# Optimization experiments

Hardware: AMD Instinct MI355X
Metric: run time of the kernel (lower is better)

## Reference

```python
import jax, jax.numpy as jnp
import numpy as np

B, T, IN_DIM, OUT_DIM = 1024, 64, 8, 2
H, K, HIDDEN = 3, 5, 256
LOG_STD_MIN, LOG_STD_MAX = -20.0, 2.0


def setup_inputs() -> dict:
    key = jax.random.key(0)
    ks = jax.random.split(key, 12)
    def lin(k, fan_in, fan_out):
        b = 1.0 / np.sqrt(fan_in)
        return jax.random.uniform(k, (fan_in, fan_out), jnp.float32, -b, b)
    inp = {
        'state': jax.random.normal(ks[0], (B, T, IN_DIM), jnp.float32),
        'noise': jax.random.normal(ks[1], (B, T, OUT_DIM), jnp.float32),
        'Wq': lin(ks[2], IN_DIM, K * H),
        'Wk': lin(ks[3], K, K * H),
        'Wv': lin(ks[4], K, K * H),
        'W1': lin(ks[5], K * H + IN_DIM, HIDDEN),
        'b1': jnp.zeros((HIDDEN,), jnp.float32),
        'W2': lin(ks[6], HIDDEN, HIDDEN),
        'b2': jnp.zeros((HIDDEN,), jnp.float32),
        'Wmu': jax.random.uniform(ks[7], (HIDDEN, OUT_DIM), jnp.float32, -0.003, 0.003),
        'bmu': jax.random.uniform(ks[8], (OUT_DIM,), jnp.float32, -0.003, 0.003),
        'Wls': jax.random.uniform(ks[9], (HIDDEN, OUT_DIM), jnp.float32, -0.003, 0.003),
        'bls': jax.random.uniform(ks[10], (OUT_DIM,), jnp.float32, -0.003, 0.003),
    }
    return inp


# static off-diagonal neighbor indices: row i -> all j != i
_OFFDIAG = np.array([[j for j in range(T) if j != i] for i in range(T)], dtype=np.int32)


def _forward(state, noise, Wq, Wk, Wv, W1, b1, W2, b2, Wmu, bmu, Wls, bls):
    b, t, _ = state.shape
    # rel[b,i,j] = state[b,j,:4] - state[b,i,:4]
    rel4 = state[:, None, :, 0:4] - state[:, :, None, 0:4]          # [b,t,t,4] (x,y,vx,vy)
    x_comp = rel4[..., 0::2]                                         # [x, vx]
    y_comp = rel4[..., 1::2]                                         # [y, vy]
    ang = (-state[:, :, 7] + 0.5 * jnp.pi)[:, None, :, None]         # varies with j (own-ref of key agent)
    c, s = jnp.cos(ang), jnp.sin(ang)
    xn = x_comp * c - y_comp * s                                     # [x', vx']
    yn = x_comp * s + y_comp * c                                     # [y', vy']
    rel = jnp.stack([xn[..., 0], yn[..., 0], xn[..., 1], yn[..., 1]], axis=-1)  # [b,t,t,4]
    # drop self-pairs (diagonal) -> [b,t,t-1,4]
    idx = jnp.asarray(_OFFDIAG)
    rel_od = rel[:, jnp.arange(t)[:, None], idx]
    r = jnp.sqrt(rel_od[..., 0] ** 2 + rel_od[..., 1] ** 2)[..., None]   # [b,t,t-1,1]
    r_trans = jax.nn.sigmoid(1.0 - 5.0 * (r - 0.2))                       # 1/(1+exp(-1+5(r-0.2)))
    rel_n = jnp.concatenate([rel_od[..., 0:2] / r, rel_od[..., 2:4], r_trans], axis=-1)  # [b,t,t-1,5]
    h, k = H, K
    q = (state @ Wq).reshape(b, t, h, k)                              # [b,t,h,k]
    keys = (rel_n @ Wk).reshape(b, t, t - 1, h, k)                    # [b,t,n,h,k]
    vals = (rel_n @ Wv).reshape(b, t, t - 1, h, k)
    scores = jnp.einsum('btnhk,bthk->bthn', keys, q) / jnp.sqrt(jnp.float32(k))
    w = jax.nn.softmax(scores, axis=-1)                               # over t-1 neighbors
    att = jnp.einsum('bthn,btnhk->bthk', w, vals).reshape(b, t, h * k)
    x = jnp.concatenate([att, state], axis=-1)
    x = jax.nn.relu(x @ W1 + b1)
    x = jax.nn.relu(x @ W2 + b2)
    mu = jnp.tanh(x @ Wmu + bmu)
    log_std = jnp.tanh(x @ Wls + bls)
    log_std = LOG_STD_MIN + 0.5 * (LOG_STD_MAX - LOG_STD_MIN) * (log_std + 1.0)
    std = jnp.exp(log_std)
    z = mu + std * noise                                              # rsample with explicit noise
    action = jnp.tanh(z)
    # Normal(mu,std).log_prob(z) with (z-mu)/std == noise
    log_prob = -0.5 * noise ** 2 - log_std - 0.5 * jnp.log(2.0 * jnp.pi)
    log_prob = log_prob - jnp.log(1.0 - action ** 2 + 1e-7)
    log_prob = jnp.sum(log_prob, axis=-1, keepdims=True)
    return action, log_prob


def reference(state, noise, Wq, Wk, Wv, W1, b1, W2, b2, Wmu, bmu, Wls, bls):
    return _forward(state, noise, Wq, Wk, Wv, W1, b1, W2, b2, Wmu, bmu, Wls, bls)
```

## Files before the change

kernel.cpp:

```cpp
#include <hip/hip_runtime.h>
#include <math.h>

#define NROWS 65536

typedef short bf16x8 __attribute__((ext_vector_type(8)));
typedef float f32x4  __attribute__((ext_vector_type(4)));
typedef float f32x2  __attribute__((ext_vector_type(2)));
typedef unsigned int u32x2 __attribute__((ext_vector_type(2)));

__device__ __forceinline__ unsigned short f2bf(float x){
    unsigned int u = __float_as_uint(x);
    u += 0x7FFFu + ((u >> 16) & 1u);
    return (unsigned short)(u >> 16);
}
__device__ __forceinline__ unsigned int pkbf(float lo, float hi){
    unsigned int r;
    asm("v_cvt_pk_bf16_f32 %0, %1, %2" : "=v"(r) : "v"(lo), "v"(hi));
    return r;
}
__device__ __forceinline__ f32x2 sp2(float x){ return (f32x2){x, x}; }

template<int CTRL, int RM>
__device__ __forceinline__ float dpp_add(float v){
    int m = __builtin_amdgcn_update_dpp(0, __float_as_int(v), CTRL, RM, 0xF, 1);
    return v + __int_as_float(m);
}
__device__ __forceinline__ float bfly8_add(float v){
    v = dpp_add<0xB1, 0xF>(v);
    v = dpp_add<0x4E, 0xF>(v);
    v = dpp_add<0x141, 0xF>(v);
    return v;
}
__device__ __forceinline__ float red4_lq(float v){
    v += __int_as_float(__builtin_amdgcn_ds_swizzle(__float_as_int(v), 0x401F));
    v += __shfl_xor(v, 32, 64);
    return v;
}
__device__ __forceinline__ float fast_tanh(float x){
    float e = __builtin_amdgcn_exp2f(x * 2.8853900817779268f);
    return 1.f - 2.f * __builtin_amdgcn_rcpf(e + 1.f);
}

__global__ __launch_bounds__(256) void prep_kernel(
    const float* __restrict__ W2, const float* __restrict__ W1,
    unsigned short* __restrict__ w2frag, unsigned short* __restrict__ w1frag)
{
    const int bx = blockIdx.x, t = threadIdx.x;
    if (bx < 128){
        const int ct = bx >> 3, kk = bx & 7;
        #pragma unroll
        for (int s = 0; s < 2; ++s){
            int f = t * 2 + s;
            int lane = f >> 3, e = f & 7;
            int k = kk * 32 + (lane >> 4) * 8 + e;
            int c = ct * 16 + (lane & 15);
            w2frag[(size_t)(ct * 8 + kk) * 512 + f] = f2bf(W2[k * 256 + c]);
        }
    } else {
        #pragma unroll
        for (int s = 0; s < 32; ++s){
            int flat = t * 32 + s;
            int ct = flat >> 9, r = flat & 511;
            int lane = r >> 3, e = r & 7;
            int k = (lane >> 4) * 8 + e;
            int c = ct * 16 + (lane & 15);
            w1frag[flat] = (k < 23) ? f2bf(W1[k * 256 + c]) : (unsigned short)0;
        }
    }
}

__global__ __launch_bounds__(512, 4) void actor_kernel(
    const float* __restrict__ state, const float* __restrict__ noise,
    const float* __restrict__ Wq, const float* __restrict__ Wk,
    const float* __restrict__ Wv,
    const unsigned short* __restrict__ w1frag, const float* __restrict__ b1,
    const unsigned short* __restrict__ w2frag, const float* __restrict__ b2,
    const float* __restrict__ Wmu, const float* __restrict__ bmu,
    const float* __restrict__ Wls, const float* __restrict__ bls,
    float* __restrict__ action_out, float* __restrict__ logprob_out)
{
    __shared__ __align__(16) unsigned char uniA[64 * 264 * 2];
    float* sLDS  = (float*)uniA;
    float* pjLDS = sLDS + 576;
    float* qkLDS = pjLDS + 384;
    unsigned short* h1LDS = (unsigned short*)uniA;
    __shared__ __align__(16) unsigned short x0LDS[64 * 40];
    __shared__ __align__(16) float headLDS[8 * 64 * 4];

    const int t    = threadIdx.x;
    const int lane = t & 63;
    const int w    = t >> 6;
    const int lm   = lane & 15;
    const int lq   = lane >> 4;
    const int b    = blockIdx.x;

    {
        float v = state[(size_t)b * 512 + t];
        int r = t >> 3, c = t & 7;
        sLDS[r * 9 + c] = v;
        if (c < 4) pjLDS[(r & 31) * 12 + c * 2 + (r >> 5)] = v;
    }
    __syncthreads();

    if (t < 192){
        const int row = t & 63, h = t >> 6;
        float s[8];
        #pragma unroll
        for (int d = 0; d < 8; ++d) s[d] = sLDS[row * 9 + d];
        float q[5];
        #pragma unroll
        for (int e = 0; e < 5; ++e){
            int m = h * 5 + e;
            float acc = 0.f;
            #pragma unroll
            for (int d = 0; d < 8; ++d) acc += s[d] * Wq[d * 15 + m];
            q[e] = acc;
        }
        #pragma unroll
        for (int f = 0; f < 5; ++f){
            float acc = 0.f;
            #pragma unroll
            for (int kk = 0; kk < 5; ++kk) acc += Wk[f * 15 + h * 5 + kk] * q[kk];
            qkLDS[row * 20 + h * 5 + f] = acc * 0.64519834f;
        }
    } else if (w == 7){
        const int row = lane;
        float ang = 1.5707963267948966f - sLDS[row * 9 + 7];
        float sn, cs;
        __sincosf(ang, &sn, &cs);
        int base = (row & 31) * 12 + (row >> 5);
        pjLDS[base + 8]  = sn;
        pjLDS[base + 10] = cs;
    }
    __syncthreads();

    {
        const int il = lane >> 3;
        const int js = lane & 7;
        const int i  = w * 8 + il;
        const float si0 = sLDS[i * 9 + 0], si1 = sLDS[i * 9 + 1];
        const float si2 = sLDS[i * 9 + 2], si3 = sLDS[i * 9 + 3];
        float qkv[16];
        *(f32x4*)&qkv[0]  = *(const f32x4*)&qkLDS[i * 20 + 0];
        *(f32x4*)&qkv[4]  = *(const f32x4*)&qkLDS[i * 20 + 4];
        *(f32x4*)&qkv[8]  = *(const f32x4*)&qkLDS[i * 20 + 8];
        *(f32x4*)&qkv[12] = *(const f32x4*)&qkLDS[i * 20 + 12];

        f32x2 s0 = {0.f,0.f}, s1 = {0.f,0.f}, s2 = {0.f,0.f};
        f32x2 g0[5], g1[5], g2[5];
        #pragma unroll
        for (int f = 0; f < 5; ++f){ g0[f] = sp2(0.f); g1[f] = sp2(0.f); g2[f] = sp2(0.f); }

        #pragma unroll
        for (int jj = 0; jj < 4; ++jj){
            const int jb = jj * 8 + js;
            const f32x2* pp = (const f32x2*)&pjLDS[jb * 12];
            f32x2 p0 = pp[0], p1 = pp[1], p2 = pp[2], p3 = pp[3];
            f32x2 sn = pp[4], cs = pp[5];
            f32x2 d0 = p0 - sp2(si0), d1 = p1 - sp2(si1);
            f32x2 d2 = p2 - sp2(si2), d3 = p3 - sp2(si3);
            f32x2 xn0 = d0 * cs - d1 * sn, yn0 = d0 * sn + d1 * cs;
            f32x2 xn1 = d2 * cs - d3 * sn, yn1 = d2 * sn + d3 * cs;
            f32x2 r2v = xn0 * xn0 + yn0 * yn0;
            const bool self0 = (jb == i), self1 = (jb + 32 == i);
            f32x2 inv_r;
            inv_r.x = self0 ? 0.f : __builtin_amdgcn_rsqf(r2v.x);
            inv_r.y = self1 ? 0.f : __builtin_amdgcn_rsqf(r2v.y);
            f32x2 rv  = r2v * inv_r;
            f32x2 arg = rv * sp2(7.2134752f) - sp2(2.8853901f);
            f32x2 f4;
            f4.x = __builtin_amdgcn_rcpf(1.f + __builtin_amdgcn_exp2f(arg.x));
            f4.y = __builtin_amdgcn_rcpf(1.f + __builtin_amdgcn_exp2f(arg.y));
            f32x2 f0 = xn0 * inv_r, f1 = yn0 * inv_r;
            f32x2 sc0 = f0*sp2(qkv[0])  + f1*sp2(qkv[1])  + xn1*sp2(qkv[2])  + yn1*sp2(qkv[3])  + f4*sp2(qkv[4]);
            f32x2 sc1 = f0*sp2(qkv[5])  + f1*sp2(qkv[6])  + xn1*sp2(qkv[7])  + yn1*sp2(qkv[8])  + f4*sp2(qkv[9]);
            f32x2 sc2 = f0*sp2(qkv[10]) + f1*sp2(qkv[11]) + xn1*sp2(qkv[12]) + yn1*sp2(qkv[13]) + f4*sp2(qkv[14]);
            f32x2 e0, e1, e2;
            e0.x = self0 ? 0.f : __builtin_amdgcn_exp2f(sc0.x);  e0.y = self1 ? 0.f : __builtin_amdgcn_exp2f(sc0.y);
            e1.x = self0 ? 0.f : __builtin_amdgcn_exp2f(sc1.x);  e1.y = self1 ? 0.f : __builtin_amdgcn_exp2f(sc1.y);
            e2.x = self0 ? 0.f : __builtin_amdgcn_exp2f(sc2.x);  e2.y = self1 ? 0.f : __builtin_amdgcn_exp2f(sc2.y);
            s0 += e0; s1 += e1; s2 += e2;
            g0[0] += e0*f0; g0[1] += e0*f1; g0[2] += e0*xn1; g0[3] += e0*yn1; g0[4] += e0*f4;
            g1[0] += e1*f0; g1[1] += e1*f1; g1[2] += e1*xn1; g1[3] += e1*yn1; g1[4] += e1*f4;
            g2[0] += e2*f0; g2[1] += e2*f1; g2[2] += e2*xn1; g2[3] += e2*yn1; g2[4] += e2*f4;
        }
        float S0 = s0.x + s0.y, S1 = s1.x + s1.y, S2 = s2.x + s2.y;
        float G0[5], G1[5], G2[5];
        #pragma unroll
        for (int f = 0; f < 5; ++f){
            G0[f] = bfly8_add(g0[f].x + g0[f].y);
            G1[f] = bfly8_add(g1[f].x + g1[f].y);
            G2[f] = bfly8_add(g2[f].x + g2[f].y);
        }
        S0 = bfly8_add(S0); S1 = bfly8_add(S1); S2 = bfly8_add(S2);
        float i0 = __builtin_amdgcn_rcpf(S0);
        float i1 = __builtin_amdgcn_rcpf(S1);
        float i2 = __builtin_amdgcn_rcpf(S2);

        #pragma unroll
        for (int mm = 0; mm < 2; ++mm){
            int m = js * 2 + mm;
            if (m < 15){
                float A0 = (m < 5) ? G0[0] : (m < 10) ? G1[0] : G2[0];
                float A1 = (m < 5) ? G0[1] : (m < 10) ? G1[1] : G2[1];
                float A2 = (m < 5) ? G0[2] : (m < 10) ? G1[2] : G2[2];
                float A3 = (m < 5) ? G0[3] : (m < 10) ? G1[3] : G2[3];
                float A4 = (m < 5) ? G0[4] : (m < 10) ? G1[4] : G2[4];
                float I  = (m < 5) ? i0    : (m < 10) ? i1    : i2;
                float av = (A0 * Wv[m] + A1 * Wv[15 + m] + A2 * Wv[30 + m]
                          + A3 * Wv[45 + m] + A4 * Wv[60 + m]) * I;
                x0LDS[i * 40 + m] = f2bf(av);
            }
        }
        x0LDS[i * 40 + 15 + js] = f2bf(sLDS[i * 9 + js]);
        x0LDS[i * 40 + 23 + js] = 0;
        if (js == 0) x0LDS[i * 40 + 31] = 0;
    }
    __syncthreads();

    {
        bf16x8 afr[4];
        #pragma unroll
        for (int rt = 0; rt < 4; ++rt)
            afr[rt] = *(const bf16x8*)&x0LDS[(rt * 16 + lm) * 40 + lq * 8];
        #pragma unroll
        for (int ci = 0; ci < 2; ++ci){
            const int ct = w * 2 + ci;
            bf16x8 bfr = *(const bf16x8*)&w1frag[(size_t)ct * 512 + lane * 8];
            f32x4 bb = *(const f32x4*)&b1[ct * 16 + lq * 4];
            #pragma unroll
            for (int rt = 0; rt < 4; ++rt){
                f32x4 c0 = {0.f, 0.f, 0.f, 0.f};
                c0 = __builtin_amdgcn_mfma_f32_16x16x32_bf16(bfr, afr[rt], c0, 0, 0, 0);
                float h0 = fmaxf(c0[0] + bb[0], 0.f);
                float h1v = fmaxf(c0[1] + bb[1], 0.f);
                float h2v = fmaxf(c0[2] + bb[2], 0.f);
                float h3v = fmaxf(c0[3] + bb[3], 0.f);
                u32x2 pk; pk.x = pkbf(h0, h1v); pk.y = pkbf(h2v, h3v);
                *(u32x2*)&h1LDS[(rt * 16 + lm) * 264 + ct * 16 + lq * 4] = pk;
            }
        }
    }
    __syncthreads();

    {
        f32x4 acc[4][2];
        #pragma unroll
        for (int rt = 0; rt < 4; ++rt)
            #pragma unroll
            for (int ci = 0; ci < 2; ++ci) acc[rt][ci] = (f32x4){0.f, 0.f, 0.f, 0.f};

        #pragma unroll
        for (int kk = 0; kk < 8; ++kk){
            bf16x8 arf[4], brf[2];
            #pragma unroll
            for (int rt = 0; rt < 4; ++rt)
                arf[rt] = *(const bf16x8*)&h1LDS[(rt * 16 + lm) * 264 + kk * 32 + lq * 8];
            #pragma unroll
            for (int ci = 0; ci < 2; ++ci)
                brf[ci] = *(const bf16x8*)&w2frag[(size_t)((w * 2 + ci) * 8 + kk) * 512 + lane * 8];
            #pragma unroll
            for (int rt = 0; rt < 4; ++rt)
                #pragma unroll
                for (int ci = 0; ci < 2; ++ci)
                    acc[rt][ci] = __builtin_amdgcn_mfma_f32_16x16x32_bf16(brf[ci], arf[rt], acc[rt][ci], 0, 0, 0);
        }
        f32x4 b2v[2], wmA[2], wmB[2], wlA[2], wlB[2];
        #pragma unroll
        for (int ci = 0; ci < 2; ++ci){
            int cb = (w * 2 + ci) * 16 + lq * 4;
            b2v[ci] = *(const f32x4*)&b2[cb];
            wmA[ci] = *(const f32x4*)&Wmu[cb * 2];
            wmB[ci] = *(const f32x4*)&Wmu[cb * 2 + 4];
            wlA[ci] = *(const f32x4*)&Wls[cb * 2];
            wlB[ci] = *(const f32x4*)&Wls[cb * 2 + 4];
        }
        #pragma unroll
        for (int rt = 0; rt < 4; ++rt){
            float m0 = 0.f, m1 = 0.f, l0 = 0.f, l1 = 0.f;
            #pragma unroll
            for (int ci = 0; ci < 2; ++ci){
                float hv0 = fmaxf(acc[rt][ci][0] + b2v[ci][0], 0.f);
                float hv1 = fmaxf(acc[rt][ci][1] + b2v[ci][1], 0.f);
                float hv2 = fmaxf(acc[rt][ci][2] + b2v[ci][2], 0.f);
                float hv3 = fmaxf(acc[rt][ci][3] + b2v[ci][3], 0.f);
                m0 += hv0*wmA[ci][0] + hv1*wmA[ci][2] + hv2*wmB[ci][0] + hv3*wmB[ci][2];
                m1 += hv0*wmA[ci][1] + hv1*wmA[ci][3] + hv2*wmB[ci][1] + hv3*wmB[ci][3];
                l0 += hv0*wlA[ci][0] + hv1*wlA[ci][2] + hv2*wlB[ci][0] + hv3*wlB[ci][2];
                l1 += hv0*wlA[ci][1] + hv1*wlA[ci][3] + hv2*wlB[ci][1] + hv3*wlB[ci][3];
            }
            m0 = red4_lq(m0); m1 = red4_lq(m1);
            l0 = red4_lq(l0); l1 = red4_lq(l1);
            if (lq == 0){
                f32x4 o = {m0, m1, l0, l1};
                *(f32x4*)&headLDS[(w * 64 + rt * 16 + lm) * 4] = o;
            }
        }
    }
    __syncthreads();

    if (t < 64){
        const int row = t;
        f32x4 s = {0.f, 0.f, 0.f, 0.f};
        #pragma unroll
        for (int ww = 0; ww < 8; ++ww)
            s += *(const f32x4*)&headLDS[(ww * 64 + row) * 4];
        const size_t grow = (size_t)b * 64 + row;
        float n0 = noise[grow * 2 + 0];
        float n1 = noise[grow * 2 + 1];
        float lp = 0.f;
        {
            float mu = fast_tanh(s[0] + bmu[0]);
            float ls = fast_tanh(s[2] + bls[0]);
            ls = -20.f + 11.f * (ls + 1.f);
            float sd = __builtin_amdgcn_exp2f(ls * 1.4426950408889634f);
            float a = fast_tanh(mu + sd * n0);
            action_out[grow * 2 + 0] = a;
            lp += -0.5f * n0 * n0 - ls - 0.9189385332046727f
                - 0.6931471805599453f * __builtin_amdgcn_logf(1.f - a * a + 1e-7f);
        }
        {
            float mu = fast_tanh(s[1] + bmu[1]);
            float ls = fast_tanh(s[3] + bls[1]);
            ls = -20.f + 11.f * (ls + 1.f);
            float sd = __builtin_amdgcn_exp2f(ls * 1.4426950408889634f);
            float a = fast_tanh(mu + sd * n1);
            action_out[grow * 2 + 1] = a;
            lp += -0.5f * n1 * n1 - ls - 0.9189385332046727f
                - 0.6931471805599453f * __builtin_amdgcn_logf(1.f - a * a + 1e-7f);
        }
        logprob_out[grow] = lp;
    }
}

extern "C" void kernel_launch(void* const* d_in, const int* in_sizes, int n_in,
                              void* d_out, int out_size, void* d_ws, size_t ws_size,
                              hipStream_t stream)
{
    (void)in_sizes; (void)n_in; (void)out_size; (void)ws_size;
    const float* state = (const float*)d_in[0];
    const float* noise = (const float*)d_in[1];
    const float* Wq  = (const float*)d_in[2];
    const float* Wk  = (const float*)d_in[3];
    const float* Wv  = (const float*)d_in[4];
    const float* W1  = (const float*)d_in[5];
    const float* b1  = (const float*)d_in[6];
    const float* W2  = (const float*)d_in[7];
    const float* b2  = (const float*)d_in[8];
    const float* Wmu = (const float*)d_in[9];
    const float* bmu = (const float*)d_in[10];
    const float* Wls = (const float*)d_in[11];
    const float* bls = (const float*)d_in[12];

    unsigned short* w2frag = (unsigned short*)d_ws;
    unsigned short* w1frag = w2frag + 65536;

    float* action_out  = (float*)d_out;
    float* logprob_out = (float*)d_out + (size_t)NROWS * 2;

    prep_kernel<<<129, 256, 0, stream>>>(W2, W1, w2frag, w1frag);
    actor_kernel<<<1024, 512, 0, stream>>>(state, noise, Wq, Wk, Wv,
        w1frag, b1, w2frag, b2, Wmu, bmu, Wls, bls, action_out, logprob_out);
}
```

Measured before the change: 110.9 us.

## Fold Wq·Wk into a precomputed matrix, drop a barrier, raise occupancy

The weight-only product Wq·Wkᵀ, scaled, is computed once in the prep kernel, so each block needs one 8-wide dot per query-key feature instead of two chained small matmuls. The query and sincos work now reads state straight from global memory, which removes one __syncthreads. Distance is taken from the unrotated deltas with a small epsilon in place of the self-pair select before rsq. Launch bounds go from 4 to 6 waves per SIMD, and a sched_barrier after the MFMA loop constrains instruction scheduling, which may cost register spills.

New measurement: 118.7 us. +7.0%, slower.

```diff
diff --git a/kernel.cpp b/kernel.cpp
--- a/kernel.cpp
+++ b/kernel.cpp
@@ -43,7 +43,9 @@
 
 __global__ __launch_bounds__(256) void prep_kernel(
     const float* __restrict__ W2, const float* __restrict__ W1,
-    unsigned short* __restrict__ w2frag, unsigned short* __restrict__ w1frag)
+    const float* __restrict__ Wq, const float* __restrict__ Wk,
+    unsigned short* __restrict__ w2frag, unsigned short* __restrict__ w1frag,
+    float* __restrict__ Cqk)
 {
     const int bx = blockIdx.x, t = threadIdx.x;
     if (bx < 128){
@@ -56,7 +58,7 @@
             int c = ct * 16 + (lane & 15);
             w2frag[(size_t)(ct * 8 + kk) * 512 + f] = f2bf(W2[k * 256 + c]);
         }
-    } else {
+    } else if (bx == 128){
         #pragma unroll
         for (int s = 0; s < 32; ++s){
             int flat = t * 32 + s;
@@ -66,12 +68,21 @@
             int c = ct * 16 + (lane & 15);
             w1frag[flat] = (k < 23) ? f2bf(W1[k * 256 + c]) : (unsigned short)0;
         }
-    }
-}
-
-__global__ __launch_bounds__(512, 4) void actor_kernel(
+    } else {
+        if (t < 120){
+            int h = t / 40, rem = t % 40, f = rem >> 3, d = rem & 7;
+            float acc = 0.f;
+            #pragma unroll
+            for (int kk = 0; kk < 5; ++kk)
+                acc += Wk[f * 15 + h * 5 + kk] * Wq[d * 15 + h * 5 + kk];
+            Cqk[t] = acc * 0.64519834f;
+        }
+    }
+}
+
+__global__ __launch_bounds__(512, 6) void actor_kernel(
     const float* __restrict__ state, const float* __restrict__ noise,
-    const float* __restrict__ Wq, const float* __restrict__ Wk,
+    const float* __restrict__ Cqk,
     const float* __restrict__ Wv,
     const unsigned short* __restrict__ w1frag, const float* __restrict__ b1,
     const unsigned short* __restrict__ w2frag, const float* __restrict__ b2,
@@ -99,38 +110,29 @@
         int r = t >> 3, c = t & 7;
         sLDS[r * 9 + c] = v;
         if (c < 4) pjLDS[(r & 31) * 12 + c * 2 + (r >> 5)] = v;
-    }
-    __syncthreads();
-
-    if (t < 192){
-        const int row = t & 63, h = t >> 6;
-        float s[8];
-        #pragma unroll
-        for (int d = 0; d < 8; ++d) s[d] = sLDS[row * 9 + d];
-        float q[5];
-        #pragma unroll
-        for (int e = 0; e < 5; ++e){
-            int m = h * 5 + e;
-            float acc = 0.f;
-            #pragma unroll
-            for (int d = 0; d < 8; ++d) acc += s[d] * Wq[d * 15 + m];
-            q[e] = acc;
-        }
-        #pragma unroll
-        for (int f = 0; f < 5; ++f){
-            float acc = 0.f;
-            #pragma unroll
-            for (int kk = 0; kk < 5; ++kk) acc += Wk[f * 15 + h * 5 + kk] * q[kk];
-            qkLDS[row * 20 + h * 5 + f] = acc * 0.64519834f;
-        }
-    } else if (w == 7){
-        const int row = lane;
-        float ang = 1.5707963267948966f - sLDS[row * 9 + 7];
-        float sn, cs;
-        __sincosf(ang, &sn, &cs);
-        int base = (row & 31) * 12 + (row >> 5);
-        pjLDS[base + 8]  = sn;
-        pjLDS[base + 10] = cs;
+
+        if (t < 192){
+            const int row = t & 63, h = t >> 6;
+            f32x4 sA = *(const f32x4*)&state[(size_t)b * 512 + row * 8];
+            f32x4 sB = *(const f32x4*)&state[(size_t)b * 512 + row * 8 + 4];
+            #pragma unroll
+            for (int f = 0; f < 5; ++f){
+                const float* cp = &Cqk[(h * 5 + f) * 8];
+                f32x4 cA = *(const f32x4*)cp;
+                f32x4 cB = *(const f32x4*)(cp + 4);
+                float acc = sA[0]*cA[0] + sA[1]*cA[1] + sA[2]*cA[2] + sA[3]*cA[3]
+                          + sB[0]*cB[0] + sB[1]*cB[1] + sB[2]*cB[2] + sB[3]*cB[3];
+                qkLDS[row * 20 + h * 5 + f] = acc;
+            }
+        } else if (w == 7){
+            const int row = lane;
+            float ang = 1.5707963267948966f - state[(size_t)b * 512 + row * 8 + 7];
+            float sn, cs;
+            __sincosf(ang, &sn, &cs);
+            int base = (row & 31) * 12 + (row >> 5);
+            pjLDS[base + 8]  = sn;
+            pjLDS[base + 10] = cs;
+        }
     }
     __syncthreads();
 
@@ -159,13 +161,12 @@
             f32x2 sn = pp[4], cs = pp[5];
             f32x2 d0 = p0 - sp2(si0), d1 = p1 - sp2(si1);
             f32x2 d2 = p2 - sp2(si2), d3 = p3 - sp2(si3);
+            f32x2 r2v = d0 * d0 + d1 * d1 + sp2(1e-30f);
             f32x2 xn0 = d0 * cs - d1 * sn, yn0 = d0 * sn + d1 * cs;
             f32x2 xn1 = d2 * cs - d3 * sn, yn1 = d2 * sn + d3 * cs;
-            f32x2 r2v = xn0 * xn0 + yn0 * yn0;
-            const bool self0 = (jb == i), self1 = (jb + 32 == i);
             f32x2 inv_r;
-            inv_r.x = self0 ? 0.f : __builtin_amdgcn_rsqf(r2v.x);
-            inv_r.y = self1 ? 0.f : __builtin_amdgcn_rsqf(r2v.y);
+            inv_r.x = __builtin_amdgcn_rsqf(r2v.x);
+            inv_r.y = __builtin_amdgcn_rsqf(r2v.y);
             f32x2 rv  = r2v * inv_r;
             f32x2 arg = rv * sp2(7.2134752f) - sp2(2.8853901f);
             f32x2 f4;
@@ -175,6 +176,7 @@
             f32x2 sc0 = f0*sp2(qkv[0])  + f1*sp2(qkv[1])  + xn1*sp2(qkv[2])  + yn1*sp2(qkv[3])  + f4*sp2(qkv[4]);
             f32x2 sc1 = f0*sp2(qkv[5])  + f1*sp2(qkv[6])  + xn1*sp2(qkv[7])  + yn1*sp2(qkv[8])  + f4*sp2(qkv[9]);
             f32x2 sc2 = f0*sp2(qkv[10]) + f1*sp2(qkv[11]) + xn1*sp2(qkv[12]) + yn1*sp2(qkv[13]) + f4*sp2(qkv[14]);
+            const bool self0 = (jb == i), self1 = (jb + 32 == i);
             f32x2 e0, e1, e2;
             e0.x = self0 ? 0.f : __builtin_amdgcn_exp2f(sc0.x);  e0.y = self1 ? 0.f : __builtin_amdgcn_exp2f(sc0.y);
             e1.x = self0 ? 0.f : __builtin_amdgcn_exp2f(sc1.x);  e1.y = self1 ? 0.f : __builtin_amdgcn_exp2f(sc1.y);
@@ -265,6 +267,8 @@
                 for (int ci = 0; ci < 2; ++ci)
                     acc[rt][ci] = __builtin_amdgcn_mfma_f32_16x16x32_bf16(brf[ci], arf[rt], acc[rt][ci], 0, 0, 0);
         }
+        __builtin_amdgcn_sched_barrier(0);
+
         f32x4 b2v[2], wmA[2], wmB[2], wlA[2], wlB[2];
         #pragma unroll
         for (int ci = 0; ci < 2; ++ci){
@@ -354,11 +358,12 @@
 
     unsigned short* w2frag = (unsigned short*)d_ws;
     unsigned short* w1frag = w2frag + 65536;
+    float* Cqk = (float*)(w1frag + 8192);
 
     float* action_out  = (float*)d_out;
     float* logprob_out = (float*)d_out + (size_t)NROWS * 2;
 
-    prep_kernel<<<129, 256, 0, stream>>>(W2, W1, w2frag, w1frag);
-    actor_kernel<<<1024, 512, 0, stream>>>(state, noise, Wq, Wk, Wv,
+    prep_kernel<<<130, 256, 0, stream>>>(W2, W1, Wq, Wk, w2frag, w1frag, Cqk);
+    actor_kernel<<<1024, 512, 0, stream>>>(state, noise, Cqk, Wv,
         w1frag, b1, w2frag, b2, Wmu, bmu, Wls, bls, action_out, logprob_out);
 }
```
